# Kernel optimization log

Hardware: AMD Instinct MI355X
Metric: run time of the kernel (lower is better)

## Reference

```python
import jax, jax.numpy as jnp
import numpy as np

L, H, P = 32768, 256, 256
DT_MIN, DT_MAX = 0.001, 0.1


def setup_inputs() -> dict:
    key = jax.random.key(0)
    ks = jax.random.split(key, 7)
    signal = jax.random.normal(ks[0], (L, H), jnp.float32)
    # stable HiPPO-like init: negative real part, random imaginary part
    lam_re = -(0.1 + 0.4 * jax.random.uniform(ks[1], (P,), jnp.float32))
    lam_im = jax.random.normal(ks[2], (P,), jnp.float32)
    Lambda_ri = jnp.stack([lam_re, lam_im], axis=-1)            # (P, 2)
    B_ri = jax.random.normal(ks[3], (P, H, 2), jnp.float32) / np.float32(np.sqrt(H))
    C_ri = jax.random.normal(ks[4], (H, P, 2), jnp.float32) / np.float32(np.sqrt(P))
    D = jax.random.uniform(ks[5], (H,), jnp.float32)
    log_step = jnp.log(DT_MIN + (DT_MAX - DT_MIN) * jax.random.uniform(ks[6], (P,), jnp.float32))
    return {"signal": signal, "Lambda_ri": Lambda_ri, "B_ri": B_ri,
            "C_ri": C_ri, "D": D, "log_step": log_step}


def reference(signal, Lambda_ri, B_ri, C_ri, D, log_step):
    # --- get_BC_tilde (bcInit='dense'): B stored real (P,H,2) -> complex ---
    Lambda = jax.lax.complex(Lambda_ri[..., 0], Lambda_ri[..., 1])   # (P,)
    B_tilde = jax.lax.complex(B_ri[..., 0], B_ri[..., 1])            # (P, H)
    C_tilde = jax.lax.complex(C_ri[..., 0], C_ri[..., 1])            # (H, P)

    # --- discretize_zoh ---
    step = jnp.exp(log_step)                                          # (P,) step_scale = 1.0
    Lambda_bar = jnp.exp(Lambda * step)                               # (P,) complex
    B_bar = ((Lambda_bar - 1.0) / Lambda)[:, None] * B_tilde          # (P, H) complex

    # --- apply_ssm: Bu_elements = vmap(u -> B_bar @ u) over time ---
    Bu = signal.astype(Lambda_bar.dtype) @ B_bar.T                    # (L, P) complex
    Lam = jnp.broadcast_to(Lambda_bar, Bu.shape)                      # (L, P)

    def binop(qi, qj):
        A_i, Bu_i = qi
        A_j, Bu_j = qj
        return (A_j * A_i, Bu_j + A_j * Bu_i)

    _, xs = jax.lax.associative_scan(binop, (Lam, Bu), axis=0)        # (L, P)

    # y = Re(C_tilde @ x) + D * u, vectorized over time
    y = jnp.real(xs @ C_tilde.T) + D * signal                         # (L, H)
    return y
```

## Files before the change

### kernel.cpp

```cpp
#include <hip/hip_runtime.h>
#include <math.h>

constexpr int L = 32768;
constexpr int H = 256;
constexpr int P = 256;
constexpr int T = 64;
constexpr int NC = L / T;
constexpr int N1 = 2 * P;
constexpr int LDEP = 130;

typedef __attribute__((ext_vector_type(8))) short short8;
typedef __attribute__((ext_vector_type(4))) float f32x4;

__device__ __forceinline__ unsigned f2bf(float f) {
  unsigned u = __float_as_uint(f);
  return (u + 0x7FFFu + ((u >> 16) & 1u)) >> 16;
}
__device__ __forceinline__ float bf_lo(unsigned u) { return __uint_as_float(u << 16); }
__device__ __forceinline__ float bf_hi(unsigned u) { return __uint_as_float(u & 0xFFFF0000u); }

__device__ __forceinline__ void lambda_bar_of(const float* __restrict__ lam,
                                              const float* __restrict__ lstep,
                                              int p, float& lbr, float& lbi) {
  float lr = lam[2 * p], li = lam[2 * p + 1];
  float st = expf(lstep[p]);
  float ea = expf(lr * st);
  lbr = ea * cosf(li * st);
  lbi = ea * sinf(li * st);
}

__device__ __forceinline__ unsigned fix2(unsigned w, float pr, float pi, float cr, float ci) {
  float xgr = fmaf(pr, cr, fmaf(-pi, ci, bf_lo(w)));
  float xgi = fmaf(pr, ci, fmaf(pi, cr, bf_hi(w)));
  return f2bf(xgr) | (f2bf(xgi) << 16);
}


__global__ __launch_bounds__(256) void k_prep(const float* __restrict__ sig,
                                              const float* __restrict__ lam,
                                              const float* __restrict__ lstep,
                                              const float* __restrict__ Bri,
                                              const float* __restrict__ Cri,
                                              unsigned short* __restrict__ Asw,
                                              unsigned short* __restrict__ Bsw,
                                              unsigned short* __restrict__ Csw,
                                              float* __restrict__ powsw) {
  __shared__ __align__(16) unsigned short plds[16 * 272];
  const int tid = threadIdx.x, bx = blockIdx.x;
  if (bx < 2048) {
    const float4* sig4 = (const float4*)sig;
    size_t fb = (size_t)bx * 1024;
#pragma unroll
    for (int u = 0; u < 4; u++) {
      int idx = u * 256 + tid;
      float4 a = sig4[fb + idx];
      int row = idx >> 6, colf = (idx & 63) * 4;
      uint2 w;
      w.x = f2bf(a.x) | (f2bf(a.y) << 16);
      w.y = f2bf(a.z) | (f2bf(a.w) << 16);
      *(uint2*)(plds + row * 272 + colf) = w;
    }
    __syncthreads();
    uint4* dst = (uint4*)Asw + (size_t)bx * 512;
#pragma unroll
    for (int u = 0; u < 2; u++) {
      int s = u * 256 + tid;
      int kb = s >> 6, ln = s & 63;
      int row = ln & 15, k0 = kb * 32 + (ln >> 4) * 8;
      dst[s] = *(const uint4*)(plds + row * 272 + k0);
    }
    return;
  }
  if (bx < 2112) {
    int o = (bx - 2048) * 256 + tid;
    int slab = o >> 6, ln = o & 63;
    int n16 = slab >> 3, kb = slab & 7;
    int n = n16 * 16 + (ln & 15);
    int k0 = kb * 32 + (ln >> 4) * 8;
    int p = n >> 1, comp = n & 1;
    float lr = lam[2 * p], li = lam[2 * p + 1];
    float st = expf(lstep[p]);
    float ea = expf(lr * st);
    float lbr = ea * cosf(li * st), lbi = ea * sinf(li * st);
    float inv = 1.0f / (lr * lr + li * li);
    float nr = lbr - 1.0f;
    float fr = (nr * lr + lbi * li) * inv, fi = (lbi * lr - nr * li) * inv;
    unsigned wv[4];
#pragma unroll
    for (int m = 0; m < 4; m++) {
      unsigned lh[2];
#pragma unroll
      for (int h2 = 0; h2 < 2; h2++) {
        int k = k0 + m * 2 + h2;
        float br = Bri[2 * (p * H + k)], bi = Bri[2 * (p * H + k) + 1];
        float v = comp ? (fr * bi + fi * br) : (fr * br - fi * bi);
        lh[h2] = f2bf(v);
      }
      wv[m] = lh[0] | (lh[1] << 16);
    }
    uint4 w; w.x = wv[0]; w.y = wv[1]; w.z = wv[2]; w.w = wv[3];
    ((uint4*)Bsw)[o] = w;
    return;
  }
  if (bx < 2176) {
    int o = (bx - 2112) * 256 + tid;
    int slab = o >> 6, ln = o & 63;
    int h16 = slab >> 4, kb = slab & 15;
    int h = h16 * 16 + (ln & 15);
    int k0 = kb * 32 + (ln >> 4) * 8;
    unsigned wv[4];
#pragma unroll
    for (int m = 0; m < 4; m++) {
      unsigned lh[2];
#pragma unroll
      for (int h2 = 0; h2 < 2; h2++) {
        int kcat = k0 + m * 2 + h2;
        int p = kcat >> 1;
        float v = (kcat & 1) ? -Cri[2 * (h * P + p) + 1] : Cri[2 * (h * P + p)];
        lh[h2] = f2bf(v);
      }
      wv[m] = lh[0] | (lh[1] << 16);
    }
    uint4 w; w.x = wv[0]; w.y = wv[1]; w.z = wv[2]; w.w = wv[3];
    ((uint4*)Csw)[o] = w;
    return;
  }
  {
    int o = (bx - 2176) * 256 + tid;
    int s = o >> 1, half = o & 1;
    int ln = s & 63, slab = s >> 6;
    int t16 = slab >> 4, kb = slab & 15;
    int t = t16 * 16 + (ln & 15);
    int kbase = kb * 32 + (ln >> 4) * 8 + half * 4;
    float e = (float)(t + 1);
    float4 v;
    {
      int p = kbase >> 1;
      float lr = lam[2 * p], li = lam[2 * p + 1], st = expf(lstep[p]);
      float er = expf(e * lr * st);
      v.x = er * cosf(e * li * st);
      v.y = er * sinf(e * li * st);
    }
    {
      int p = (kbase >> 1) + 1;
      float lr = lam[2 * p], li = lam[2 * p + 1], st = expf(lstep[p]);
      float er = expf(e * lr * st);
      v.z = er * cosf(e * li * st);
      v.w = er * sinf(e * li * st);
    }
    ((float4*)powsw)[o] = v;
  }
}

__global__ __launch_bounds__(256) void k_gemm1(const unsigned short* __restrict__ Asw,
                                               const unsigned short* __restrict__ Bsw,
                                               const float* __restrict__ lam,
                                               const float* __restrict__ lstep,
                                               unsigned short* __restrict__ Xsw,
                                               float* __restrict__ Sr,
                                               float* __restrict__ Si) {
  __shared__ __align__(16) float sEpi[T * LDEP];
  const int tid = threadIdx.x, lane = tid & 63, wave = tid >> 6;
  const int wr = (wave & 1) * 32, wc = (wave >> 1) * 64;
  const int c = blockIdx.y, n0 = blockIdx.x * 128;
  const unsigned short* Ab = Asw + ((size_t)(c * 4 + (wr >> 4)) * 8) * 512 + lane * 8;
  const unsigned short* Bb = Bsw + ((size_t)((n0 + wc) >> 4) * 8) * 512 + lane * 8;
  f32x4 acc[2][4];
#pragma unroll
  for (int i = 0; i < 2; i++)
#pragma unroll
    for (int j = 0; j < 4; j++) acc[i][j] = (f32x4){0.f, 0.f, 0.f, 0.f};

#pragma unroll 4
  for (int kb = 0; kb < 8; kb++) {
    short8 af[2], bf[4];
    af[0] = *(const short8*)(Ab + kb * 512);
    af[1] = *(const short8*)(Ab + 8 * 512 + kb * 512);
#pragma unroll
    for (int j = 0; j < 4; j++) bf[j] = *(const short8*)(Bb + j * 8 * 512 + kb * 512);
#pragma unroll
    for (int i = 0; i < 2; i++)
#pragma unroll
      for (int j = 0; j < 4; j++)
        acc[i][j] = __builtin_amdgcn_mfma_f32_16x16x32_bf16(af[i], bf[j], acc[i][j], 0, 0, 0);
  }

  const int crow = (lane >> 4) * 4, ccol = lane & 15;
#pragma unroll
  for (int i = 0; i < 2; i++)
#pragma unroll
    for (int j = 0; j < 4; j++)
#pragma unroll
      for (int g = 0; g < 4; g++)
        sEpi[(wr + i * 16 + crow + g) * LDEP + (wc + j * 16 + ccol)] = acc[i][j][g];
  __syncthreads();

  if (tid < 64) {
    const int pl = tid;
    const int gp = (n0 >> 1) + pl;
    float lbr, lbi;
    lambda_bar_of(lam, lstep, gp, lbr, lbi);
    const int kbx = (n0 >> 5) + (pl >> 4);
    const int slot16 = 16 * ((pl >> 2) & 3);
    const int off2 = (pl & 3) * 2;
    float xr = 0.f, xi = 0.f;
    const float* e = sEpi + 2 * pl;
    for (int tb = 0; tb < T; tb += 8) {
      float2 v[8];
#pragma unroll
      for (int u = 0; u < 8; u++) v[u] = *(const float2*)(e + (tb + u) * LDEP);
      unsigned ov[8];
#pragma unroll
      for (int u = 0; u < 8; u++) {
        float nr = fmaf(lbr, xr, fmaf(-lbi, xi, v[u].x));
        float ni = fmaf(lbr, xi, fmaf(lbi, xr, v[u].y));
        xr = nr; xi = ni;
        ov[u] = f2bf(xr) | (f2bf(xi) << 16);
      }
      size_t slabbase = ((size_t)(c * 4 + (tb >> 4)) * 16 + kbx) * 512;
#pragma unroll
      for (int u = 0; u < 8; u++)
        *(unsigned*)(Xsw + slabbase + ((tb & 15) + u + slot16) * 8 + off2) = ov[u];
    }
    Sr[c * P + gp] = xr;
    Si[c * P + gp] = xi;
  }
}

__global__ __launch_bounds__(256) void k_carry(const float* __restrict__ lam,
                                               const float* __restrict__ lstep,
                                               const float* __restrict__ Sr,
                                               const float* __restrict__ Si,
                                               float* __restrict__ carcat) {
  const int p = threadIdx.x;
  float lr = lam[2 * p], li = lam[2 * p + 1];
  float st = expf(lstep[p]);
  float ea = expf((float)T * lr * st);
  float lTr = ea * cosf((float)T * li * st);
  float lTi = ea * sinf((float)T * li * st);
  float cr = 0.f, ci = 0.f;
  for (int c0 = 0; c0 < NC; c0 += 32) {
    float vr[32], vi[32];
#pragma unroll
    for (int u = 0; u < 32; u++) {
      vr[u] = Sr[(c0 + u) * P + p];
      vi[u] = Si[(c0 + u) * P + p];
    }
#pragma unroll
    for (int u = 0; u < 32; u++) {
      *(float2*)(carcat + (size_t)(c0 + u) * N1 + 2 * p) = make_float2(cr, ci);
      float nr = fmaf(lTr, cr, fmaf(-lTi, ci, vr[u]));
      float ni = fmaf(lTr, ci, fmaf(lTi, cr, vi[u]));
      cr = nr; ci = ni;
    }
  }
}

__global__ __launch_bounds__(256) void k_gemm2(const unsigned short* __restrict__ Xsw,
                                               const unsigned short* __restrict__ Csw,
                                               const float* __restrict__ powsw,
                                               const float* __restrict__ carcat,
                                               const float* __restrict__ sig,
                                               const float* __restrict__ Dv,
                                               float* __restrict__ out) {
  const int tid = threadIdx.x, lane = tid & 63, wave = tid >> 6;
  const int wr = (wave & 1) * 32, wc = (wave >> 1) * 64;
  const int c = blockIdx.y, n0 = blockIdx.x * 128;
  const int m0 = c * 64;
  const unsigned short* Ab = Xsw + ((size_t)(c * 4 + (wr >> 4)) * 16) * 512 + lane * 8;
  const unsigned short* Bb = Csw + ((size_t)((n0 + wc) >> 4) * 16) * 512 + lane * 8;
  const float* Pw = powsw + ((size_t)(wr >> 4) * 16) * 512 + lane * 8;
  const float* Cw = carcat + (size_t)c * N1 + (lane >> 4) * 8;
  f32x4 acc[2][4];
#pragma unroll
  for (int i = 0; i < 2; i++)
#pragma unroll
    for (int j = 0; j < 4; j++) acc[i][j] = (f32x4){0.f, 0.f, 0.f, 0.f};

#pragma unroll 2
  for (int kb = 0; kb < 16; kb++) {
    uint4 x0 = *(const uint4*)(Ab + kb * 512);
    uint4 x1 = *(const uint4*)(Ab + 16 * 512 + kb * 512);
    float4 pa0 = *(const float4*)(Pw + kb * 512);
    float4 pb0 = *(const float4*)(Pw + kb * 512 + 4);
    float4 pa1 = *(const float4*)(Pw + 16 * 512 + kb * 512);
    float4 pb1 = *(const float4*)(Pw + 16 * 512 + kb * 512 + 4);
    float4 ca = *(const float4*)(Cw + kb * 32);
    float4 cb = *(const float4*)(Cw + kb * 32 + 4);
    short8 bf[4];
#pragma unroll
    for (int j = 0; j < 4; j++) bf[j] = *(const short8*)(Bb + j * 16 * 512 + kb * 512);
    union { short8 s; uint4 u; } A0, A1;
    A0.u.x = fix2(x0.x, pa0.x, pa0.y, ca.x, ca.y);
    A0.u.y = fix2(x0.y, pa0.z, pa0.w, ca.z, ca.w);
    A0.u.z = fix2(x0.z, pb0.x, pb0.y, cb.x, cb.y);
    A0.u.w = fix2(x0.w, pb0.z, pb0.w, cb.z, cb.w);
    A1.u.x = fix2(x1.x, pa1.x, pa1.y, ca.x, ca.y);
    A1.u.y = fix2(x1.y, pa1.z, pa1.w, ca.z, ca.w);
    A1.u.z = fix2(x1.z, pb1.x, pb1.y, cb.x, cb.y);
    A1.u.w = fix2(x1.w, pb1.z, pb1.w, cb.z, cb.w);
#pragma unroll
    for (int j = 0; j < 4; j++) {
      acc[0][j] = __builtin_amdgcn_mfma_f32_16x16x32_bf16(A0.s, bf[j], acc[0][j], 0, 0, 0);
      acc[1][j] = __builtin_amdgcn_mfma_f32_16x16x32_bf16(A1.s, bf[j], acc[1][j], 0, 0, 0);
    }
  }

  const int crow = (lane >> 4) * 4, ccol = lane & 15;
  float dcol[4];
#pragma unroll
  for (int j = 0; j < 4; j++) dcol[j] = Dv[n0 + wc + ccol + j * 16];
#pragma unroll
  for (int i = 0; i < 2; i++)
#pragma unroll
    for (int j = 0; j < 4; j++) {
      int col = n0 + wc + ccol + j * 16;
#pragma unroll
      for (int g = 0; g < 4; g++) {
        int row = m0 + wr + i * 16 + crow + g;
        out[(size_t)row * H + col] = acc[i][j][g] + dcol[j] * sig[(size_t)row * H + col];
      }
    }
}

extern "C" void kernel_launch(void* const* d_in, const int* in_sizes, int n_in,
                              void* d_out, int out_size, void* d_ws, size_t ws_size,
                              hipStream_t stream) {
  const float* sig = (const float*)d_in[0];
  const float* lam = (const float*)d_in[1];
  const float* Bri = (const float*)d_in[2];
  const float* Cri = (const float*)d_in[3];
  const float* Dv  = (const float*)d_in[4];
  const float* lst = (const float*)d_in[5];
  float* out = (float*)d_out;

  unsigned short* Asw = (unsigned short*)d_ws;
  unsigned short* Xsw = Asw + (size_t)L * H;
  unsigned short* Bsw = Xsw + (size_t)L * N1;
  unsigned short* Csw = Bsw + (size_t)N1 * H;
  float* powsw  = (float*)(Csw + (size_t)H * N1);
  float* Sr     = powsw + 64 * 512;
  float* Si     = Sr + NC * P;
  float* carcat = Si + NC * P;

  k_prep<<<2208, 256, 0, stream>>>(sig, lam, lst, Bri, Cri, Asw, Bsw, Csw, powsw);
  dim3 g1(N1 / 128, NC);
  k_gemm1<<<g1, 256, 0, stream>>>(Asw, Bsw, lam, lst, Xsw, Sr, Si);
  k_carry<<<1, 256, 0, stream>>>(lam, lst, Sr, Si, carcat);
  dim3 g2(H / 128, NC);
  k_gemm2<<<g2, 256, 0, stream>>>(Xsw, Csw, powsw, carcat, sig, Dv, out);
}
```

Measured before the change: 175.1 us.

## Parallelize chunk-carry scan across waves and shrink GEMM tiles for more blocks

The serial single-block carry recurrence over 512 chunks is replaced by one 64-thread block per state, each thread scanning 8 chunks locally and then combining results with a wave-level shuffle-based associative scan. Both GEMM kernels drop from 128-column to 64-column tiles, with each wave owning 16 rows, which doubles the block count. The aim is to remove the long serial carry latency and to raise occupancy and parallelism in the GEMMs. In exchange, operand reuse per block falls, and the scan recomputes complex powers in fp32, which may change rounding slightly.

```diff
diff --git a/kernel.cpp b/kernel.cpp
--- a/kernel.cpp
+++ b/kernel.cpp
@@ -7,7 +7,7 @@
 constexpr int T = 64;
 constexpr int NC = L / T;
 constexpr int N1 = 2 * P;
-constexpr int LDEP = 130;
+constexpr int LDEP = 66;
 
 typedef __attribute__((ext_vector_type(8))) short short8;
 typedef __attribute__((ext_vector_type(4))) float f32x4;
@@ -161,41 +161,33 @@
                                                float* __restrict__ Si) {
   __shared__ __align__(16) float sEpi[T * LDEP];
   const int tid = threadIdx.x, lane = tid & 63, wave = tid >> 6;
-  const int wr = (wave & 1) * 32, wc = (wave >> 1) * 64;
-  const int c = blockIdx.y, n0 = blockIdx.x * 128;
-  const unsigned short* Ab = Asw + ((size_t)(c * 4 + (wr >> 4)) * 8) * 512 + lane * 8;
-  const unsigned short* Bb = Bsw + ((size_t)((n0 + wc) >> 4) * 8) * 512 + lane * 8;
-  f32x4 acc[2][4];
-#pragma unroll
-  for (int i = 0; i < 2; i++)
-#pragma unroll
-    for (int j = 0; j < 4; j++) acc[i][j] = (f32x4){0.f, 0.f, 0.f, 0.f};
-
-#pragma unroll 4
+  const int c = blockIdx.y, n0 = blockIdx.x * 64;
+  const unsigned short* Ab = Asw + ((size_t)(c * 4 + wave) * 8) * 512 + lane * 8;
+  const unsigned short* Bb = Bsw + ((size_t)(n0 >> 4) * 8) * 512 + lane * 8;
+  f32x4 acc[4];
+#pragma unroll
+  for (int j = 0; j < 4; j++) acc[j] = (f32x4){0.f, 0.f, 0.f, 0.f};
+
+#pragma unroll
   for (int kb = 0; kb < 8; kb++) {
-    short8 af[2], bf[4];
-    af[0] = *(const short8*)(Ab + kb * 512);
-    af[1] = *(const short8*)(Ab + 8 * 512 + kb * 512);
+    short8 af = *(const short8*)(Ab + kb * 512);
+    short8 bf[4];
 #pragma unroll
     for (int j = 0; j < 4; j++) bf[j] = *(const short8*)(Bb + j * 8 * 512 + kb * 512);
 #pragma unroll
-    for (int i = 0; i < 2; i++)
-#pragma unroll
-      for (int j = 0; j < 4; j++)
-        acc[i][j] = __builtin_amdgcn_mfma_f32_16x16x32_bf16(af[i], bf[j], acc[i][j], 0, 0, 0);
+    for (int j = 0; j < 4; j++)
+      acc[j] = __builtin_amdgcn_mfma_f32_16x16x32_bf16(af, bf[j], acc[j], 0, 0, 0);
   }
 
   const int crow = (lane >> 4) * 4, ccol = lane & 15;
 #pragma unroll
-  for (int i = 0; i < 2; i++)
-#pragma unroll
-    for (int j = 0; j < 4; j++)
-#pragma unroll
-      for (int g = 0; g < 4; g++)
-        sEpi[(wr + i * 16 + crow + g) * LDEP + (wc + j * 16 + ccol)] = acc[i][j][g];
+  for (int j = 0; j < 4; j++)
+#pragma unroll
+    for (int g = 0; g < 4; g++)
+      sEpi[(wave * 16 + crow + g) * LDEP + (j * 16 + ccol)] = acc[j][g];
   __syncthreads();
 
-  if (tid < 64) {
+  if (tid < 32) {
     const int pl = tid;
     const int gp = (n0 >> 1) + pl;
     float lbr, lbi;
@@ -227,32 +219,54 @@
   }
 }
 
-__global__ __launch_bounds__(256) void k_carry(const float* __restrict__ lam,
+__global__ __launch_bounds__(64) void k_carry2(const float* __restrict__ lam,
                                                const float* __restrict__ lstep,
                                                const float* __restrict__ Sr,
                                                const float* __restrict__ Si,
                                                float* __restrict__ carcat) {
-  const int p = threadIdx.x;
+  const int p = blockIdx.x;
+  const int t = threadIdx.x;
   float lr = lam[2 * p], li = lam[2 * p + 1];
   float st = expf(lstep[p]);
-  float ea = expf((float)T * lr * st);
-  float lTr = ea * cosf((float)T * li * st);
-  float lTi = ea * sinf((float)T * li * st);
-  float cr = 0.f, ci = 0.f;
-  for (int c0 = 0; c0 < NC; c0 += 32) {
-    float vr[32], vi[32];
-#pragma unroll
-    for (int u = 0; u < 32; u++) {
-      vr[u] = Sr[(c0 + u) * P + p];
-      vi[u] = Si[(c0 + u) * P + p];
-    }
-#pragma unroll
-    for (int u = 0; u < 32; u++) {
-      *(float2*)(carcat + (size_t)(c0 + u) * N1 + 2 * p) = make_float2(cr, ci);
-      float nr = fmaf(lTr, cr, fmaf(-lTi, ci, vr[u]));
-      float ni = fmaf(lTr, ci, fmaf(lTi, cr, vi[u]));
-      cr = nr; ci = ni;
-    }
+  float eT = expf((float)T * lr * st);
+  float lTr = eT * cosf((float)T * li * st);
+  float lTi = eT * sinf((float)T * li * st);
+  float vr[8], vi[8];
+#pragma unroll
+  for (int u = 0; u < 8; u++) {
+    vr[u] = Sr[(t * 8 + u) * P + p];
+    vi[u] = Si[(t * 8 + u) * P + p];
+  }
+  float Br = 0.f, Bi = 0.f;
+#pragma unroll
+  for (int u = 0; u < 8; u++) {
+    float nr = fmaf(lTr, Br, fmaf(-lTi, Bi, vr[u]));
+    float ni = fmaf(lTr, Bi, fmaf(lTi, Br, vi[u]));
+    Br = nr; Bi = ni;
+  }
+  float e8 = expf(8.0f * (float)T * lr * st);
+  float Ar = e8 * cosf(8.0f * (float)T * li * st);
+  float Ai = e8 * sinf(8.0f * (float)T * li * st);
+#pragma unroll
+  for (int d = 1; d < 64; d <<= 1) {
+    float Aor = __shfl_up(Ar, d), Aoi = __shfl_up(Ai, d);
+    float Bor = __shfl_up(Br, d), Boi = __shfl_up(Bi, d);
+    if (t >= d) {
+      float nBr = Ar * Bor - Ai * Boi + Br;
+      float nBi = Ar * Boi + Ai * Bor + Bi;
+      float nAr = Aor * Ar - Aoi * Ai;
+      float nAi = Aor * Ai + Aoi * Ar;
+      Br = nBr; Bi = nBi; Ar = nAr; Ai = nAi;
+    }
+  }
+  float cr = __shfl_up(Br, 1), ci = __shfl_up(Bi, 1);
+  if (t == 0) { cr = 0.f; ci = 0.f; }
+#pragma unroll
+  for (int u = 0; u < 8; u++) {
+    *(float2*)(carcat + (size_t)(t * 8 + u) * N1 + 2 * p) = make_float2(cr, ci);
+    float nr = fmaf(lTr, cr, fmaf(-lTi, ci, vr[u]));
+    float ni = fmaf(lTr, ci, fmaf(lTi, cr, vi[u]));
+    cr = nr; ci = ni;
   }
 }
 
@@ -264,63 +278,49 @@
                                                const float* __restrict__ Dv,
                                                float* __restrict__ out) {
   const int tid = threadIdx.x, lane = tid & 63, wave = tid >> 6;
-  const int wr = (wave & 1) * 32, wc = (wave >> 1) * 64;
-  const int c = blockIdx.y, n0 = blockIdx.x * 128;
+  const int c = blockIdx.y, n0 = blockIdx.x * 64;
   const int m0 = c * 64;
-  const unsigned short* Ab = Xsw + ((size_t)(c * 4 + (wr >> 4)) * 16) * 512 + lane * 8;
-  const unsigned short* Bb = Csw + ((size_t)((n0 + wc) >> 4) * 16) * 512 + lane * 8;
-  const float* Pw = powsw + ((size_t)(wr >> 4) * 16) * 512 + lane * 8;
+  const unsigned short* Ab = Xsw + ((size_t)(c * 4 + wave) * 16) * 512 + lane * 8;
+  const unsigned short* Bb = Csw + ((size_t)(n0 >> 4) * 16) * 512 + lane * 8;
+  const float* Pw = powsw + ((size_t)wave * 16) * 512 + lane * 8;
   const float* Cw = carcat + (size_t)c * N1 + (lane >> 4) * 8;
-  f32x4 acc[2][4];
-#pragma unroll
-  for (int i = 0; i < 2; i++)
-#pragma unroll
-    for (int j = 0; j < 4; j++) acc[i][j] = (f32x4){0.f, 0.f, 0.f, 0.f};
-
-#pragma unroll 2
+  f32x4 acc[4];
+#pragma unroll
+  for (int j = 0; j < 4; j++) acc[j] = (f32x4){0.f, 0.f, 0.f, 0.f};
+
+#pragma unroll 4
   for (int kb = 0; kb < 16; kb++) {
     uint4 x0 = *(const uint4*)(Ab + kb * 512);
-    uint4 x1 = *(const uint4*)(Ab + 16 * 512 + kb * 512);
-    float4 pa0 = *(const float4*)(Pw + kb * 512);
-    float4 pb0 = *(const float4*)(Pw + kb * 512 + 4);
-    float4 pa1 = *(const float4*)(Pw + 16 * 512 + kb * 512);
-    float4 pb1 = *(const float4*)(Pw + 16 * 512 + kb * 512 + 4);
+    float4 pa = *(const float4*)(Pw + kb * 512);
+    float4 pb = *(const float4*)(Pw + kb * 512 + 4);
     float4 ca = *(const float4*)(Cw + kb * 32);
     float4 cb = *(const float4*)(Cw + kb * 32 + 4);
     short8 bf[4];
 #pragma unroll
     for (int j = 0; j < 4; j++) bf[j] = *(const short8*)(Bb + j * 16 * 512 + kb * 512);
-    union { short8 s; uint4 u; } A0, A1;
-    A0.u.x = fix2(x0.x, pa0.x, pa0.y, ca.x, ca.y);
-    A0.u.y = fix2(x0.y, pa0.z, pa0.w, ca.z, ca.w);
-    A0.u.z = fix2(x0.z, pb0.x, pb0.y, cb.x, cb.y);
-    A0.u.w = fix2(x0.w, pb0.z, pb0.w, cb.z, cb.w);
-    A1.u.x = fix2(x1.x, pa1.x, pa1.y, ca.x, ca.y);
-    A1.u.y = fix2(x1.y, pa1.z, pa1.w, ca.z, ca.w);
-    A1.u.z = fix2(x1.z, pb1.x, pb1.y, cb.x, cb.y);
-    A1.u.w = fix2(x1.w, pb1.z, pb1.w, cb.z, cb.w);
-#pragma unroll
-    for (int j = 0; j < 4; j++) {
-      acc[0][j] = __builtin_amdgcn_mfma_f32_16x16x32_bf16(A0.s, bf[j], acc[0][j], 0, 0, 0);
-      acc[1][j] = __builtin_amdgcn_mfma_f32_16x16x32_bf16(A1.s, bf[j], acc[1][j], 0, 0, 0);
-    }
+    union { short8 s; uint4 u; } A0;
+    A0.u.x = fix2(x0.x, pa.x, pa.y, ca.x, ca.y);
+    A0.u.y = fix2(x0.y, pa.z, pa.w, ca.z, ca.w);
+    A0.u.z = fix2(x0.z, pb.x, pb.y, cb.x, cb.y);
+    A0.u.w = fix2(x0.w, pb.z, pb.w, cb.z, cb.w);
+#pragma unroll
+    for (int j = 0; j < 4; j++)
+      acc[j] = __builtin_amdgcn_mfma_f32_16x16x32_bf16(A0.s, bf[j], acc[j], 0, 0, 0);
   }
 
   const int crow = (lane >> 4) * 4, ccol = lane & 15;
   float dcol[4];
 #pragma unroll
-  for (int j = 0; j < 4; j++) dcol[j] = Dv[n0 + wc + ccol + j * 16];
-#pragma unroll
-  for (int i = 0; i < 2; i++)
-#pragma unroll
-    for (int j = 0; j < 4; j++) {
-      int col = n0 + wc + ccol + j * 16;
-#pragma unroll
-      for (int g = 0; g < 4; g++) {
-        int row = m0 + wr + i * 16 + crow + g;
-        out[(size_t)row * H + col] = acc[i][j][g] + dcol[j] * sig[(size_t)row * H + col];
-      }
-    }
+  for (int j = 0; j < 4; j++) dcol[j] = Dv[n0 + ccol + j * 16];
+#pragma unroll
+  for (int j = 0; j < 4; j++) {
+    int col = n0 + ccol + j * 16;
+#pragma unroll
+    for (int g = 0; g < 4; g++) {
+      int row = m0 + wave * 16 + crow + g;
+      out[(size_t)row * H + col] = acc[j][g] + dcol[j] * sig[(size_t)row * H + col];
+    }
+  }
 }
 
 extern "C" void kernel_launch(void* const* d_in, const int* in_sizes, int n_in,
@@ -344,9 +344,9 @@
   float* carcat = Si + NC * P;
 
   k_prep<<<2208, 256, 0, stream>>>(sig, lam, lst, Bri, Cri, Asw, Bsw, Csw, powsw);
-  dim3 g1(N1 / 128, NC);
+  dim3 g1(N1 / 64, NC);
   k_gemm1<<<g1, 256, 0, stream>>>(Asw, Bsw, lam, lst, Xsw, Sr, Si);
-  k_carry<<<1, 256, 0, stream>>>(lam, lst, Sr, Si, carcat);
-  dim3 g2(H / 128, NC);
+  k_carry2<<<P, 64, 0, stream>>>(lam, lst, Sr, Si, carcat);
+  dim3 g2(H / 64, NC);
   k_gemm2<<<g2, 256, 0, stream>>>(Xsw, Csw, powsw, carcat, sig, Dv, out);
 }
```

Measured after the change: 180.1 us. 1.03x slower.
